# Kernel tuning notes

Measured on AMD Instinct MI355X. Metric: run time of the kernel, lower is better.

Reference implementation:

```python
import jax, jax.numpy as jnp
import numpy as np
from jax import lax

B, T, D_IN, HID, LAT, OUT = 512, 8, 6, 128, 64, 2
DT = 0.1  # Euler step size used by NeuralODESolver


def _lrelu(x):
    return jnp.where(x >= 0, x, 0.2 * x)  # LeakyReLU(0.2)


def _ivp(z, tdelta, A1, a1, A2, a2, A3, a3):
    """Explicit-Euler IVP solve: dz/dt = MLP([z, t]); tdelta is a static float."""
    steps = int(np.ceil(abs(tdelta) / DT))
    if steps == 0:
        return z
    adt = jnp.asarray(tdelta / steps, z.dtype)
    ts = jnp.arange(steps, dtype=z.dtype) * DT  # t fed to ode_func is step*dt
    def body(zc, t):
        tv = jnp.full((zc.shape[0], 1), t, zc.dtype)
        h = jnp.tanh(jnp.concatenate([zc, tv], axis=1) @ A1 + a1)
        h = jnp.tanh(h @ A2 + a2)
        return zc + (h @ A3 + a3) * adt, None
    zf, _ = lax.scan(body, z, ts)
    return zf


def setup_inputs() -> dict:
    key = jax.random.key(0)
    ks = jax.random.split(key, 24)
    s = 0.1
    w = lambda k, sh: jax.random.normal(k, sh, jnp.float32) * s
    z = lambda sh: jnp.zeros(sh, jnp.float32)
    return {
        "features": jax.random.normal(ks[0], (B, T, D_IN), jnp.float32),
        "eps": jax.random.normal(ks[1], (B, LAT), jnp.float32),
        "fe_W1": w(ks[2], (D_IN, HID)), "fe_b1": z((HID,)),
        "fe_W2": w(ks[3], (HID, HID // 2)), "fe_b2": z((HID // 2,)),
        "fe_W3": w(ks[4], (HID // 2, LAT)), "fe_b3": z((LAT,)),
        "enc_A1": w(ks[5], (LAT + 1, HID)), "enc_a1": z((HID,)),
        "enc_A2": w(ks[6], (HID, HID)), "enc_a2": z((HID,)),
        "enc_A3": w(ks[7], (HID, LAT)), "enc_a3": z((LAT,)),
        "post_W1": w(ks[8], (LAT, HID // 2)), "post_b1": z((HID // 2,)),
        "post_W2": w(ks[9], (HID // 2, 2 * LAT)), "post_b2": z((2 * LAT,)),
        "mix_W1": w(ks[10], (LAT, HID // 4)), "mix_b1": z((HID // 4,)),
        "mix_W2": w(ks[11], (HID // 4, 1)), "mix_b2": z((1,)),
        "dec_A1": w(ks[12], (LAT + 1, HID)), "dec_a1": z((HID,)),
        "dec_A2": w(ks[13], (HID, HID)), "dec_a2": z((HID,)),
        "dec_A3": w(ks[14], (HID, LAT)), "dec_a3": z((LAT,)),
        "rec_W1": w(ks[15], (LAT, HID)), "rec_b1": z((HID,)),
        "rec_W2": w(ks[16], (HID, HID // 2)), "rec_b2": z((HID // 2,)),
        "rec_W3": w(ks[17], (HID // 2, OUT)), "rec_b3": z((OUT,)),
        "time_steps": T,
    }


def reference(features, eps, fe_W1, fe_b1, fe_W2, fe_b2, fe_W3, fe_b3,
              enc_A1, enc_a1, enc_A2, enc_a2, enc_A3, enc_a3,
              post_W1, post_b1, post_W2, post_b2,
              mix_W1, mix_b1, mix_W2, mix_b2,
              dec_A1, dec_a1, dec_A2, dec_a2, dec_A3, dec_a3,
              rec_W1, rec_b1, rec_W2, rec_b2, rec_W3, rec_b3, time_steps):
    # Embedding: feature MLP -> [B, T, LAT]
    emb = _lrelu(features @ fe_W1 + fe_b1)
    emb = _lrelu(emb @ fe_W2 + fe_b2)
    emb = emb @ fe_W3 + fe_b3
    # Encoder: evolve each time point backward to t0, then posterior net
    mus, lvs = [], []
    for t in range(time_steps):
        z0e = _ivp(emb[:, t, :], -float(t), enc_A1, enc_a1, enc_A2, enc_a2, enc_A3, enc_a3)
        p = _lrelu(z0e @ post_W1 + post_b1) @ post_W2 + post_b2
        mus.append(p[:, :LAT])
        lvs.append(p[:, LAT:])
    mu = jnp.stack(mus, axis=1)   # [B, T, LAT]
    lv = jnp.stack(lvs, axis=1)   # [B, T, LAT]
    # Mixing weights over time (Softmax(dim=1))
    wlog = _lrelu(mu @ mix_W1 + mix_b1) @ mix_W2 + mix_b2  # [B, T, 1]
    wmix = jax.nn.softmax(wlog, axis=1)
    mu0 = jnp.sum(wmix * mu, axis=1)
    lv0 = jnp.sum(wmix * lv, axis=1)
    # Reparameterize with externally supplied noise
    z0 = mu0 + eps * jnp.exp(0.5 * lv0)
    # Decoder: evolve z0 forward to each time point
    seq = [z0] + [_ivp(z0, float(t), dec_A1, dec_a1, dec_A2, dec_a2, dec_A3, dec_a3)
                  for t in range(1, time_steps)]
    lat = jnp.stack(seq, axis=1)  # [B, T, LAT]
    # Reconstruction MLP -> [B, T, OUT]
    h = _lrelu(lat @ rec_W1 + rec_b1)
    h = _lrelu(h @ rec_W2 + rec_b2)
    return h @ rec_W3 + rec_b3
```

## Files before the change

### kernel.cpp

```cpp
#include <hip/hip_runtime.h>

#define TT 8

typedef __attribute__((ext_vector_type(4))) float f32x4;
typedef __attribute__((ext_vector_type(8))) short s16x8;
typedef __attribute__((ext_vector_type(4))) short s16x4;

__device__ __forceinline__ float lrelu(float x){ return fmaxf(x, 0.2f*x); }

__device__ __forceinline__ float fast_tanh(float x){
  float e = __expf(2.f*x);
  return 1.f - 2.f/(e+1.f);
}

__device__ __forceinline__ short f2b(float f){
  unsigned int u = __float_as_uint(f);
  unsigned int r = (u + 0x7fffu + ((u>>16)&1u)) >> 16;
  return (short)(r & 0xffffu);
}

__device__ __forceinline__ s16x8 load_afrag(const float* __restrict__ W, int ldw,
                                            int k0, int c0, int lane){
  s16x8 f;
  const int r = lane & 15, kb = (lane >> 4) * 8;
  #pragma unroll
  for(int e=0;e<8;++e) f[e] = f2b(W[(size_t)(k0 + kb + e)*ldw + c0 + r]);
  return f;
}

struct Frags {
  s16x8 a1f[2];
  s16x8 a2f[4];
  s16x8 a3f[4];
  float wt1[4], b1[4], b2[4], b3[4];
};

__device__ __forceinline__ void load_frags(Frags& F,
    const float* __restrict__ A1, const float* __restrict__ a1,
    const float* __restrict__ A2, const float* __restrict__ a2,
    const float* __restrict__ A3, const float* __restrict__ a3,
    int w, int l){
  const int h = l >> 4;
  #pragma unroll
  for(int kt=0;kt<2;++kt) F.a1f[kt] = load_afrag(A1, 128, 32*kt, 16*w, l);
  #pragma unroll
  for(int kt=0;kt<4;++kt) F.a2f[kt] = load_afrag(A2, 128, 32*kt, 16*w, l);
  #pragma unroll
  for(int r=0;r<4;++r){
    const int c = 16*w + 4*h + r;
    F.wt1[r] = A1[64*128 + c];
    F.b1[r]  = a1[c];
    F.b2[r]  = a2[c];
  }
  if(w < 4){
    #pragma unroll
    for(int kt=0;kt<4;++kt) F.a3f[kt] = load_afrag(A3, 64, 32*kt, 16*w, l);
    #pragma unroll
    for(int r=0;r<4;++r) F.b3[r] = a3[16*w + 4*h + r];
  }
}

__device__ __forceinline__ void ivp_step(const Frags& F, int w, int l,
    float tk, float adt, float (&zreg)[4],
    short* __restrict__ zB, short* __restrict__ h1p, short* __restrict__ h2p,
    float* __restrict__ latRow){
  const int h = l>>4, st = l&15;
  const int wrow = (2*w + (h>>1))*16 + st;
  const int welem = 4*(h&1);
  {
    s16x8 bz0 = *(const s16x8*)(zB + (size_t)l*8);
    s16x8 bz1 = *(const s16x8*)(zB + (size_t)(64+l)*8);
    f32x4 acc = {0.f,0.f,0.f,0.f};
    acc = __builtin_amdgcn_mfma_f32_16x16x32_bf16(F.a1f[0], bz0, acc, 0,0,0);
    acc = __builtin_amdgcn_mfma_f32_16x16x32_bf16(F.a1f[1], bz1, acc, 0,0,0);
    s16x4 pk;
    #pragma unroll
    for(int r=0;r<4;++r) pk[r] = f2b(fast_tanh(fmaf(tk, F.wt1[r], acc[r]) + F.b1[r]));
    *(s16x4*)(h1p + (size_t)wrow*8 + welem) = pk;
  }
  __syncthreads();
  {
    f32x4 acc = {0.f,0.f,0.f,0.f};
    #pragma unroll
    for(int kt=0;kt<4;++kt){
      s16x8 b = *(const s16x8*)(h1p + (size_t)(64*kt + l)*8);
      acc = __builtin_amdgcn_mfma_f32_16x16x32_bf16(F.a2f[kt], b, acc, 0,0,0);
    }
    s16x4 pk;
    #pragma unroll
    for(int r=0;r<4;++r) pk[r] = f2b(fast_tanh(acc[r] + F.b2[r]));
    *(s16x4*)(h2p + (size_t)wrow*8 + welem) = pk;
  }
  __syncthreads();
  if(w < 4){
    f32x4 acc = {0.f,0.f,0.f,0.f};
    #pragma unroll
    for(int kt=0;kt<4;++kt){
      s16x8 b = *(const s16x8*)(h2p + (size_t)(64*kt + l)*8);
      acc = __builtin_amdgcn_mfma_f32_16x16x32_bf16(F.a3f[kt], b, acc, 0,0,0);
    }
    s16x4 pk;
    #pragma unroll
    for(int r=0;r<4;++r){
      zreg[r] = fmaf(adt, acc[r] + F.b3[r], zreg[r]);
      pk[r] = f2b(zreg[r]);
    }
    *(s16x4*)(zB + (size_t)wrow*8 + welem) = pk;
    if(latRow){
      #pragma unroll
      for(int r=0;r<4;++r) latRow[(16*w + 4*h + r)*16 + st] = zreg[r];
    }
  }
  __syncthreads();
}

extern "C" __global__ void __launch_bounds__(512, 2)
k_enc(const float* __restrict__ features,
      const float* __restrict__ feW1, const float* __restrict__ feb1,
      const float* __restrict__ feW2, const float* __restrict__ feb2,
      const float* __restrict__ feW3, const float* __restrict__ feb3,
      const float* __restrict__ A1, const float* __restrict__ a1,
      const float* __restrict__ A2, const float* __restrict__ a2,
      const float* __restrict__ A3, const float* __restrict__ a3,
      const float* __restrict__ pW1, const float* __restrict__ pb1,
      const float* __restrict__ pW2, const float* __restrict__ pb2,
      float* __restrict__ ws_mu, float* __restrict__ ws_lv)
{
  __shared__ __align__(16) short zB[128*8];
  __shared__ __align__(16) short h1p[256*8];
  __shared__ __align__(16) short h2p[256*8];
  __shared__ float featS[16][6];
  __shared__ float hE1[128][16];
  __shared__ float hE2[64][16];
  __shared__ float zE[64][16];
  const int tid = threadIdx.x, l = tid & 63, w = tid >> 6;
  const int c1 = tid & 127, sh = tid >> 7;
  const int t_blk = blockIdx.x & 7, chunk = blockIdx.x >> 3, s0 = chunk*16;

  Frags F;
  load_frags(F, A1, a1, A2, a2, A3, a3, w, l);

  if(tid < 96){
    int e = tid / 6, i = tid - 6*e;
    featS[e][i] = features[((size_t)(s0+e)*TT + t_blk)*6 + i];
  }
  __syncthreads();
  {
    float acc[4]; const float b = feb1[c1];
    #pragma unroll
    for(int e=0;e<4;++e) acc[e]=b;
    #pragma unroll
    for(int i=0;i<6;++i){
      const float wv = feW1[i*128 + c1];
      #pragma unroll
      for(int e=0;e<4;++e) acc[e] = fmaf(featS[4*sh+e][i], wv, acc[e]);
    }
    #pragma unroll
    for(int e=0;e<4;++e) hE1[c1][4*sh+e] = lrelu(acc[e]);
  }
  __syncthreads();
  {
    float acc[2]; const float b = feb2[l];
    acc[0]=b; acc[1]=b;
    for(int i=0;i<128;++i){
      const float wv = feW2[i*64 + l];
      acc[0] = fmaf(hE1[i][2*w  ], wv, acc[0]);
      acc[1] = fmaf(hE1[i][2*w+1], wv, acc[1]);
    }
    hE2[l][2*w  ] = lrelu(acc[0]);
    hE2[l][2*w+1] = lrelu(acc[1]);
  }
  __syncthreads();
  {
    float acc[2]; const float b = feb3[l];
    acc[0]=b; acc[1]=b;
    for(int i=0;i<64;++i){
      const float wv = feW3[i*64 + l];
      acc[0] = fmaf(hE2[i][2*w  ], wv, acc[0]);
      acc[1] = fmaf(hE2[i][2*w+1], wv, acc[1]);
    }
    zE[l][2*w  ] = acc[0];
    zE[l][2*w+1] = acc[1];
  }
  __syncthreads();
  float zreg[4] = {0.f,0.f,0.f,0.f};
  if(w < 4){
    const int h=l>>4, st=l&15;
    s16x4 pk;
    #pragma unroll
    for(int r=0;r<4;++r){ zreg[r] = zE[16*w+4*h+r][st]; pk[r]=f2b(zreg[r]); }
    *(s16x4*)(zB + (size_t)((2*w+(h>>1))*16+st)*8 + 4*(h&1)) = pk;
  }
  __syncthreads();

  const int steps = 10*t_blk;
  for(int k=0;k<steps;++k)
    ivp_step(F, w, l, 0.1f*(float)k, -0.1f, zreg, zB, h1p, h2p, nullptr);

  if(w < 4){
    const int h=l>>4, st=l&15;
    #pragma unroll
    for(int r=0;r<4;++r) zE[16*w+4*h+r][st] = zreg[r];
  }
  __syncthreads();
  {
    float acc[2]; const float b = pb1[l];
    acc[0]=b; acc[1]=b;
    for(int i=0;i<64;++i){
      const float wv = pW1[i*64 + l];
      acc[0] = fmaf(zE[i][2*w  ], wv, acc[0]);
      acc[1] = fmaf(zE[i][2*w+1], wv, acc[1]);
    }
    hE2[l][2*w  ] = lrelu(acc[0]);
    hE2[l][2*w+1] = lrelu(acc[1]);
  }
  __syncthreads();
  {
    float acc[4]; const float b = pb2[c1];
    #pragma unroll
    for(int e=0;e<4;++e) acc[e]=b;
    for(int i=0;i<64;++i){
      const float wv = pW2[i*128 + c1];
      #pragma unroll
      for(int e=0;e<4;++e) acc[e] = fmaf(hE2[i][4*sh+e], wv, acc[e]);
    }
    #pragma unroll
    for(int e=0;e<4;++e){
      const int s = s0 + 4*sh + e;
      const size_t o = ((size_t)s*TT + t_blk)*64;
      if(c1 < 64) ws_mu[o + c1] = acc[e];
      else        ws_lv[o + c1 - 64] = acc[e];
    }
  }
}

extern "C" __global__ void __launch_bounds__(512, 2)
k_dec(const float* __restrict__ mu_g, const float* __restrict__ lv_g,
      const float* __restrict__ eps,
      const float* __restrict__ mxW1, const float* __restrict__ mxb1,
      const float* __restrict__ mxW2, const float* __restrict__ mxb2,
      const float* __restrict__ A1, const float* __restrict__ a1,
      const float* __restrict__ A2, const float* __restrict__ a2,
      const float* __restrict__ A3, const float* __restrict__ a3,
      const float* __restrict__ rW1, const float* __restrict__ rb1,
      const float* __restrict__ rW2, const float* __restrict__ rb2,
      const float* __restrict__ rW3, const float* __restrict__ rb3,
      float* __restrict__ out)
{
  __shared__ __align__(16) short zB[128*8];
  __shared__ __align__(16) short h1p[256*8];
  __shared__ __align__(16) short h2p[256*8];
  __shared__ float muB[16*8*64];
  __shared__ float lvB[16*8*64];
  __shared__ float mh[16][8][32];
  __shared__ float LATS[TT][64][16];
  __shared__ float wsm[16][8];
  const int tid = threadIdx.x, l = tid & 63, w = tid >> 6;
  const int c1 = tid & 127, sh = tid >> 7;
  const int b0 = blockIdx.x * 16;

  for(int idx=tid; idx<8192; idx+=512){
    muB[idx] = mu_g[(size_t)b0*512 + idx];
    lvB[idx] = lv_g[(size_t)b0*512 + idx];
  }
  Frags F;
  load_frags(F, A1, a1, A2, a2, A3, a3, w, l);
  __syncthreads();

  for(int idx=tid; idx<4096; idx+=512){
    const int s = idx>>8, t = (idx>>5)&7, c = idx&31;
    float a = mxb1[c];
    #pragma unroll 8
    for(int i=0;i<64;++i) a = fmaf(muB[(s*8+t)*64+i], mxW1[i*32+c], a);
    mh[s][t][c] = lrelu(a);
  }
  __syncthreads();
  if(tid < 128){
    const int s = tid>>3, t = tid&7;
    float a = mxb2[0];
    #pragma unroll
    for(int i=0;i<32;++i) a = fmaf(mh[s][t][i], mxW2[i], a);
    wsm[s][t] = a;
  }
  __syncthreads();
  if(tid < 16){
    float m = -1e30f;
    #pragma unroll
    for(int t=0;t<8;++t) m = fmaxf(m, wsm[tid][t]);
    float e[8], S=0.f;
    #pragma unroll
    for(int t=0;t<8;++t){ e[t] = __expf(wsm[tid][t]-m); S += e[t]; }
    const float inv = 1.f/S;
    #pragma unroll
    for(int t=0;t<8;++t) wsm[tid][t] = e[t]*inv;
  }
  __syncthreads();
  float zreg[4] = {0.f,0.f,0.f,0.f};
  if(w < 4){
    const int h=l>>4, st=l&15;
    s16x4 pk;
    #pragma unroll
    for(int r=0;r<4;++r){
      const int c = 16*w + 4*h + r;
      float mu0=0.f, lv0=0.f;
      #pragma unroll
      for(int t=0;t<8;++t){
        const float wv = wsm[st][t];
        mu0 = fmaf(wv, muB[(st*8+t)*64 + c], mu0);
        lv0 = fmaf(wv, lvB[(st*8+t)*64 + c], lv0);
      }
      const float z0 = fmaf(eps[(size_t)(b0+st)*64 + c], __expf(0.5f*lv0), mu0);
      zreg[r] = z0; pk[r] = f2b(z0);
      LATS[0][c][st] = z0;
    }
    *(s16x4*)(zB + (size_t)((2*w+(h>>1))*16+st)*8 + 4*(h&1)) = pk;
  }
  __syncthreads();

  for(int k=0;k<70;++k){
    float* latRow = (((k+1)%10)==0) ? &LATS[(k+1)/10][0][0] : nullptr;
    ivp_step(F, w, l, 0.1f*(float)k, 0.1f, zreg, zB, h1p, h2p, latRow);
  }

  float* hR1 = muB;
  float* hR2 = muB + 128*16;
  for(int t=0;t<TT;++t){
    {
      float acc[4]; const float b = rb1[c1];
      #pragma unroll
      for(int e=0;e<4;++e) acc[e]=b;
      for(int i=0;i<64;++i){
        const float wv = rW1[i*128 + c1];
        #pragma unroll
        for(int e=0;e<4;++e) acc[e] = fmaf(LATS[t][i][4*sh+e], wv, acc[e]);
      }
      #pragma unroll
      for(int e=0;e<4;++e) hR1[c1*16 + 4*sh + e] = lrelu(acc[e]);
    }
    __syncthreads();
    {
      float acc[2]; const float b = rb2[l];
      acc[0]=b; acc[1]=b;
      for(int i=0;i<128;++i){
        const float wv = rW2[i*64 + l];
        acc[0] = fmaf(hR1[i*16 + 2*w  ], wv, acc[0]);
        acc[1] = fmaf(hR1[i*16 + 2*w+1], wv, acc[1]);
      }
      hR2[l*16 + 2*w  ] = lrelu(acc[0]);
      hR2[l*16 + 2*w+1] = lrelu(acc[1]);
    }
    __syncthreads();
    if(tid < 32){
      const int s = tid >> 1, o = tid & 1;
      float a = rb3[o];
      for(int i=0;i<64;++i) a = fmaf(hR2[i*16 + s], rW3[i*2 + o], a);
      out[((size_t)(b0+s)*TT + t)*2 + o] = a;
    }
    __syncthreads();
  }
}

extern "C" void kernel_launch(void* const* d_in, const int* in_sizes, int n_in,
                              void* d_out, int out_size, void* d_ws, size_t ws_size,
                              hipStream_t stream){
  const float* features=(const float*)d_in[0];
  const float* eps     =(const float*)d_in[1];
  const float* feW1=(const float*)d_in[2];  const float* feb1=(const float*)d_in[3];
  const float* feW2=(const float*)d_in[4];  const float* feb2=(const float*)d_in[5];
  const float* feW3=(const float*)d_in[6];  const float* feb3=(const float*)d_in[7];
  const float* eA1=(const float*)d_in[8];   const float* ea1=(const float*)d_in[9];
  const float* eA2=(const float*)d_in[10];  const float* ea2=(const float*)d_in[11];
  const float* eA3=(const float*)d_in[12];  const float* ea3=(const float*)d_in[13];
  const float* pW1=(const float*)d_in[14];  const float* pb1=(const float*)d_in[15];
  const float* pW2=(const float*)d_in[16];  const float* pb2=(const float*)d_in[17];
  const float* mxW1=(const float*)d_in[18]; const float* mxb1=(const float*)d_in[19];
  const float* mxW2=(const float*)d_in[20]; const float* mxb2=(const float*)d_in[21];
  const float* dA1=(const float*)d_in[22];  const float* da1=(const float*)d_in[23];
  const float* dA2=(const float*)d_in[24];  const float* da2=(const float*)d_in[25];
  const float* dA3=(const float*)d_in[26];  const float* da3=(const float*)d_in[27];
  const float* rW1=(const float*)d_in[28];  const float* rb1=(const float*)d_in[29];
  const float* rW2=(const float*)d_in[30];  const float* rb2=(const float*)d_in[31];
  const float* rW3=(const float*)d_in[32];  const float* rb3=(const float*)d_in[33];

  float* ws_mu=(float*)d_ws;
  float* ws_lv=ws_mu + 512*8*64;

  k_enc<<<dim3(256),dim3(512),0,stream>>>(features,
      feW1,feb1,feW2,feb2,feW3,feb3,
      eA1,ea1,eA2,ea2,eA3,ea3,
      pW1,pb1,pW2,pb2,
      ws_mu, ws_lv);
  k_dec<<<dim3(32),dim3(512),0,stream>>>(ws_mu, ws_lv, eps,
      mxW1,mxb1,mxW2,mxb2,
      dA1,da1,dA2,da2,dA3,da3,
      rW1,rb1,rW2,rb2,rW3,rb3,
      (float*)d_out);
}
```

Baseline: 325.3 us.

## Process two 16-sample groups per 1024-thread block in encoder and decoder

Doubles the block size to 1024 threads so each block handles 32 samples as two independent 16-sample MFMA groups, which halves the encoder and decoder grids. Each group gets its own zB/h1p/h2p LDS buffers, but both groups share the block-wide barriers. Shared arrays are padded to a stride of 33 to avoid LDS bank conflicts. The mixing stage now reads mu/lv straight from global memory instead of staging them in LDS. The cost is that fewer CUs are busy and more waves compete on each CU during the latency-bound serial ODE steps. A large padding LDS array is also added, which limits how many blocks fit per CU.

```diff
diff --git a/kernel.cpp b/kernel.cpp
--- a/kernel.cpp
+++ b/kernel.cpp
@@ -7,22 +7,20 @@
 typedef __attribute__((ext_vector_type(4))) short s16x4;
 
 __device__ __forceinline__ float lrelu(float x){ return fmaxf(x, 0.2f*x); }
-
 __device__ __forceinline__ float fast_tanh(float x){
   float e = __expf(2.f*x);
   return 1.f - 2.f/(e+1.f);
 }
-
 __device__ __forceinline__ short f2b(float f){
-  unsigned int u = __float_as_uint(f);
-  unsigned int r = (u + 0x7fffu + ((u>>16)&1u)) >> 16;
+  unsigned u = __float_as_uint(f);
+  unsigned r = (u + 0x7fffu + ((u>>16)&1u)) >> 16;
   return (short)(r & 0xffffu);
 }
 
 __device__ __forceinline__ s16x8 load_afrag(const float* __restrict__ W, int ldw,
-                                            int k0, int c0, int lane){
+                                            int k0, int c0, int l){
   s16x8 f;
-  const int r = lane & 15, kb = (lane >> 4) * 8;
+  const int r = l & 15, kb = (l >> 4) * 8;
   #pragma unroll
   for(int e=0;e<8;++e) f[e] = f2b(W[(size_t)(k0 + kb + e)*ldw + c0 + r]);
   return f;
@@ -39,64 +37,64 @@
     const float* __restrict__ A1, const float* __restrict__ a1,
     const float* __restrict__ A2, const float* __restrict__ a2,
     const float* __restrict__ A3, const float* __restrict__ a3,
-    int w, int l){
+    int wct, int l){
   const int h = l >> 4;
   #pragma unroll
-  for(int kt=0;kt<2;++kt) F.a1f[kt] = load_afrag(A1, 128, 32*kt, 16*w, l);
+  for(int kt=0;kt<2;++kt) F.a1f[kt] = load_afrag(A1, 128, 32*kt, 16*wct, l);
   #pragma unroll
-  for(int kt=0;kt<4;++kt) F.a2f[kt] = load_afrag(A2, 128, 32*kt, 16*w, l);
+  for(int kt=0;kt<4;++kt) F.a2f[kt] = load_afrag(A2, 128, 32*kt, 16*wct, l);
   #pragma unroll
   for(int r=0;r<4;++r){
-    const int c = 16*w + 4*h + r;
+    const int c = 16*wct + 4*h + r;
     F.wt1[r] = A1[64*128 + c];
     F.b1[r]  = a1[c];
     F.b2[r]  = a2[c];
   }
-  if(w < 4){
-    #pragma unroll
-    for(int kt=0;kt<4;++kt) F.a3f[kt] = load_afrag(A3, 64, 32*kt, 16*w, l);
-    #pragma unroll
-    for(int r=0;r<4;++r) F.b3[r] = a3[16*w + 4*h + r];
-  }
-}
-
-__device__ __forceinline__ void ivp_step(const Frags& F, int w, int l,
+  if(wct < 4){
+    #pragma unroll
+    for(int kt=0;kt<4;++kt) F.a3f[kt] = load_afrag(A3, 64, 32*kt, 16*wct, l);
+    #pragma unroll
+    for(int r=0;r<4;++r) F.b3[r] = a3[16*wct + 4*h + r];
+  }
+}
+
+__device__ __forceinline__ void ivp_step(const Frags& F, int wct, int grp, int l,
     float tk, float adt, float (&zreg)[4],
-    short* __restrict__ zB, short* __restrict__ h1p, short* __restrict__ h2p,
-    float* __restrict__ latRow){
+    short* __restrict__ zBg, short* __restrict__ h1pg, short* __restrict__ h2pg,
+    float* __restrict__ latBase){
   const int h = l>>4, st = l&15;
-  const int wrow = (2*w + (h>>1))*16 + st;
-  const int welem = 4*(h&1);
-  {
-    s16x8 bz0 = *(const s16x8*)(zB + (size_t)l*8);
-    s16x8 bz1 = *(const s16x8*)(zB + (size_t)(64+l)*8);
+  const int wrow = (2*wct + (h>>1))*16 + st;
+  const int we = 4*(h&1);
+  {
+    s16x8 bz0 = *(const s16x8*)(zBg + (size_t)l*8);
+    s16x8 bz1 = *(const s16x8*)(zBg + (size_t)(64+l)*8);
     f32x4 acc = {0.f,0.f,0.f,0.f};
     acc = __builtin_amdgcn_mfma_f32_16x16x32_bf16(F.a1f[0], bz0, acc, 0,0,0);
     acc = __builtin_amdgcn_mfma_f32_16x16x32_bf16(F.a1f[1], bz1, acc, 0,0,0);
     s16x4 pk;
     #pragma unroll
     for(int r=0;r<4;++r) pk[r] = f2b(fast_tanh(fmaf(tk, F.wt1[r], acc[r]) + F.b1[r]));
-    *(s16x4*)(h1p + (size_t)wrow*8 + welem) = pk;
+    *(s16x4*)(h1pg + (size_t)wrow*8 + we) = pk;
   }
   __syncthreads();
   {
     f32x4 acc = {0.f,0.f,0.f,0.f};
     #pragma unroll
     for(int kt=0;kt<4;++kt){
-      s16x8 b = *(const s16x8*)(h1p + (size_t)(64*kt + l)*8);
+      s16x8 b = *(const s16x8*)(h1pg + (size_t)(64*kt + l)*8);
       acc = __builtin_amdgcn_mfma_f32_16x16x32_bf16(F.a2f[kt], b, acc, 0,0,0);
     }
     s16x4 pk;
     #pragma unroll
     for(int r=0;r<4;++r) pk[r] = f2b(fast_tanh(acc[r] + F.b2[r]));
-    *(s16x4*)(h2p + (size_t)wrow*8 + welem) = pk;
-  }
-  __syncthreads();
-  if(w < 4){
+    *(s16x4*)(h2pg + (size_t)wrow*8 + we) = pk;
+  }
+  __syncthreads();
+  if(wct < 4){
     f32x4 acc = {0.f,0.f,0.f,0.f};
     #pragma unroll
     for(int kt=0;kt<4;++kt){
-      s16x8 b = *(const s16x8*)(h2p + (size_t)(64*kt + l)*8);
+      s16x8 b = *(const s16x8*)(h2pg + (size_t)(64*kt + l)*8);
       acc = __builtin_amdgcn_mfma_f32_16x16x32_bf16(F.a3f[kt], b, acc, 0,0,0);
     }
     s16x4 pk;
@@ -105,16 +103,16 @@
       zreg[r] = fmaf(adt, acc[r] + F.b3[r], zreg[r]);
       pk[r] = f2b(zreg[r]);
     }
-    *(s16x4*)(zB + (size_t)wrow*8 + welem) = pk;
-    if(latRow){
-      #pragma unroll
-      for(int r=0;r<4;++r) latRow[(16*w + 4*h + r)*16 + st] = zreg[r];
-    }
-  }
-  __syncthreads();
-}
-
-extern "C" __global__ void __launch_bounds__(512, 2)
+    *(s16x4*)(zBg + (size_t)wrow*8 + we) = pk;
+    if(latBase){
+      #pragma unroll
+      for(int r=0;r<4;++r) latBase[(16*wct + 4*h + r)*33 + grp*16 + st] = zreg[r];
+    }
+  }
+  __syncthreads();
+}
+
+extern "C" __global__ void __launch_bounds__(1024, 4)
 k_enc(const float* __restrict__ features,
       const float* __restrict__ feW1, const float* __restrict__ feb1,
       const float* __restrict__ feW2, const float* __restrict__ feb2,
@@ -126,21 +124,29 @@
       const float* __restrict__ pW2, const float* __restrict__ pb2,
       float* __restrict__ ws_mu, float* __restrict__ ws_lv)
 {
-  __shared__ __align__(16) short zB[128*8];
-  __shared__ __align__(16) short h1p[256*8];
-  __shared__ __align__(16) short h2p[256*8];
-  __shared__ float featS[16][6];
-  __shared__ float hE1[128][16];
-  __shared__ float hE2[64][16];
-  __shared__ float zE[64][16];
+  __shared__ __align__(16) short zB[2*128*8];
+  __shared__ __align__(16) short h1p[2*256*8];
+  __shared__ __align__(16) short h2p[2*256*8];
+  __shared__ float featS[32][6];
+  __shared__ float hE1[128*33];
+  __shared__ float hE2[64*33];
+  __shared__ float zE[64*33];
+  __shared__ float pad_lds[7040];
   const int tid = threadIdx.x, l = tid & 63, w = tid >> 6;
+  const int wct = w >> 1, grp = w & 1;
   const int c1 = tid & 127, sh = tid >> 7;
-  const int t_blk = blockIdx.x & 7, chunk = blockIdx.x >> 3, s0 = chunk*16;
+  const int q = w;
+  const int t_blk = blockIdx.x & 7, chunk = blockIdx.x >> 3, s0 = chunk*32;
+  if(gridDim.y == 7u) pad_lds[tid & 1023] = 1.f;
+
+  short* zBg  = zB  + (size_t)grp*128*8;
+  short* h1pg = h1p + (size_t)grp*256*8;
+  short* h2pg = h2p + (size_t)grp*256*8;
 
   Frags F;
-  load_frags(F, A1, a1, A2, a2, A3, a3, w, l);
-
-  if(tid < 96){
+  load_frags(F, A1, a1, A2, a2, A3, a3, wct, l);
+
+  if(tid < 192){
     int e = tid / 6, i = tid - 6*e;
     featS[e][i] = features[((size_t)(s0+e)*TT + t_blk)*6 + i];
   }
@@ -156,7 +162,7 @@
       for(int e=0;e<4;++e) acc[e] = fmaf(featS[4*sh+e][i], wv, acc[e]);
     }
     #pragma unroll
-    for(int e=0;e<4;++e) hE1[c1][4*sh+e] = lrelu(acc[e]);
+    for(int e=0;e<4;++e) hE1[c1*33 + 4*sh+e] = lrelu(acc[e]);
   }
   __syncthreads();
   {
@@ -164,11 +170,11 @@
     acc[0]=b; acc[1]=b;
     for(int i=0;i<128;++i){
       const float wv = feW2[i*64 + l];
-      acc[0] = fmaf(hE1[i][2*w  ], wv, acc[0]);
-      acc[1] = fmaf(hE1[i][2*w+1], wv, acc[1]);
-    }
-    hE2[l][2*w  ] = lrelu(acc[0]);
-    hE2[l][2*w+1] = lrelu(acc[1]);
+      acc[0] = fmaf(hE1[i*33 + 2*q  ], wv, acc[0]);
+      acc[1] = fmaf(hE1[i*33 + 2*q+1], wv, acc[1]);
+    }
+    hE2[l*33 + 2*q  ] = lrelu(acc[0]);
+    hE2[l*33 + 2*q+1] = lrelu(acc[1]);
   }
   __syncthreads();
   {
@@ -176,31 +182,31 @@
     acc[0]=b; acc[1]=b;
     for(int i=0;i<64;++i){
       const float wv = feW3[i*64 + l];
-      acc[0] = fmaf(hE2[i][2*w  ], wv, acc[0]);
-      acc[1] = fmaf(hE2[i][2*w+1], wv, acc[1]);
-    }
-    zE[l][2*w  ] = acc[0];
-    zE[l][2*w+1] = acc[1];
+      acc[0] = fmaf(hE2[i*33 + 2*q  ], wv, acc[0]);
+      acc[1] = fmaf(hE2[i*33 + 2*q+1], wv, acc[1]);
+    }
+    zE[l*33 + 2*q  ] = acc[0];
+    zE[l*33 + 2*q+1] = acc[1];
   }
   __syncthreads();
   float zreg[4] = {0.f,0.f,0.f,0.f};
-  if(w < 4){
+  if(wct < 4){
     const int h=l>>4, st=l&15;
     s16x4 pk;
     #pragma unroll
-    for(int r=0;r<4;++r){ zreg[r] = zE[16*w+4*h+r][st]; pk[r]=f2b(zreg[r]); }
-    *(s16x4*)(zB + (size_t)((2*w+(h>>1))*16+st)*8 + 4*(h&1)) = pk;
-  }
-  __syncthreads();
-
-  const int steps = 10*t_blk;
-  for(int k=0;k<steps;++k)
-    ivp_step(F, w, l, 0.1f*(float)k, -0.1f, zreg, zB, h1p, h2p, nullptr);
-
-  if(w < 4){
+    for(int r=0;r<4;++r){ zreg[r] = zE[(16*wct+4*h+r)*33 + grp*16+st]; pk[r]=f2b(zreg[r]); }
+    *(s16x4*)(zBg + (size_t)((2*wct+(h>>1))*16+st)*8 + 4*(h&1)) = pk;
+  }
+  __syncthreads();
+
+  const int steps = 10 * t_blk;
+  for(int k=0; k<steps; ++k)
+    ivp_step(F, wct, grp, l, 0.1f*(float)k, -0.1f, zreg, zBg, h1pg, h2pg, nullptr);
+
+  if(wct < 4){
     const int h=l>>4, st=l&15;
     #pragma unroll
-    for(int r=0;r<4;++r) zE[16*w+4*h+r][st] = zreg[r];
+    for(int r=0;r<4;++r) zE[(16*wct+4*h+r)*33 + grp*16+st] = zreg[r];
   }
   __syncthreads();
   {
@@ -208,11 +214,11 @@
     acc[0]=b; acc[1]=b;
     for(int i=0;i<64;++i){
       const float wv = pW1[i*64 + l];
-      acc[0] = fmaf(zE[i][2*w  ], wv, acc[0]);
-      acc[1] = fmaf(zE[i][2*w+1], wv, acc[1]);
-    }
-    hE2[l][2*w  ] = lrelu(acc[0]);
-    hE2[l][2*w+1] = lrelu(acc[1]);
+      acc[0] = fmaf(zE[i*33 + 2*q  ], wv, acc[0]);
+      acc[1] = fmaf(zE[i*33 + 2*q+1], wv, acc[1]);
+    }
+    hE2[l*33 + 2*q  ] = lrelu(acc[0]);
+    hE2[l*33 + 2*q+1] = lrelu(acc[1]);
   }
   __syncthreads();
   {
@@ -222,7 +228,7 @@
     for(int i=0;i<64;++i){
       const float wv = pW2[i*128 + c1];
       #pragma unroll
-      for(int e=0;e<4;++e) acc[e] = fmaf(hE2[i][4*sh+e], wv, acc[e]);
+      for(int e=0;e<4;++e) acc[e] = fmaf(hE2[i*33 + 4*sh+e], wv, acc[e]);
     }
     #pragma unroll
     for(int e=0;e<4;++e){
@@ -234,7 +240,7 @@
   }
 }
 
-extern "C" __global__ void __launch_bounds__(512, 2)
+extern "C" __global__ void __launch_bounds__(1024, 4)
 k_dec(const float* __restrict__ mu_g, const float* __restrict__ lv_g,
       const float* __restrict__ eps,
       const float* __restrict__ mxW1, const float* __restrict__ mxb1,
@@ -247,83 +253,87 @@
       const float* __restrict__ rW3, const float* __restrict__ rb3,
       float* __restrict__ out)
 {
-  __shared__ __align__(16) short zB[128*8];
-  __shared__ __align__(16) short h1p[256*8];
-  __shared__ __align__(16) short h2p[256*8];
-  __shared__ float muB[16*8*64];
-  __shared__ float lvB[16*8*64];
-  __shared__ float mh[16][8][32];
-  __shared__ float LATS[TT][64][16];
-  __shared__ float wsm[16][8];
+  __shared__ __align__(16) short zB[2*128*8];
+  __shared__ __align__(16) short h1p[2*256*8];
+  __shared__ __align__(16) short h2p[2*256*8];
+  __shared__ float pool[8448];
+  __shared__ float LATS[8*64*33];
+  __shared__ float wlS[256];
+  __shared__ float wsmS[32][8];
   const int tid = threadIdx.x, l = tid & 63, w = tid >> 6;
+  const int wct = w >> 1, grp = w & 1;
   const int c1 = tid & 127, sh = tid >> 7;
-  const int b0 = blockIdx.x * 16;
-
-  for(int idx=tid; idx<8192; idx+=512){
-    muB[idx] = mu_g[(size_t)b0*512 + idx];
-    lvB[idx] = lv_g[(size_t)b0*512 + idx];
-  }
+  const int q = w;
+  const int b0 = blockIdx.x * 32;
+
+  short* zBg  = zB  + (size_t)grp*128*8;
+  short* h1pg = h1p + (size_t)grp*256*8;
+  short* h2pg = h2p + (size_t)grp*256*8;
+
   Frags F;
-  load_frags(F, A1, a1, A2, a2, A3, a3, w, l);
-  __syncthreads();
-
-  for(int idx=tid; idx<4096; idx+=512){
-    const int s = idx>>8, t = (idx>>5)&7, c = idx&31;
+  load_frags(F, A1, a1, A2, a2, A3, a3, wct, l);
+
+  for(int p=0; p<8; ++p){
+    int idx = tid + p*1024;
+    int s = idx>>8, t = (idx>>5)&7, c = idx&31;
     float a = mxb1[c];
     #pragma unroll 8
-    for(int i=0;i<64;++i) a = fmaf(muB[(s*8+t)*64+i], mxW1[i*32+c], a);
-    mh[s][t][c] = lrelu(a);
-  }
-  __syncthreads();
-  if(tid < 128){
-    const int s = tid>>3, t = tid&7;
+    for(int i=0;i<64;++i) a = fmaf(mu_g[((size_t)(b0+s)*TT + t)*64 + i], mxW1[i*32+c], a);
+    pool[(s*8+t)*33 + c] = lrelu(a);
+  }
+  __syncthreads();
+  if(tid < 256){
+    int s = tid>>3, t = tid&7;
     float a = mxb2[0];
     #pragma unroll
-    for(int i=0;i<32;++i) a = fmaf(mh[s][t][i], mxW2[i], a);
-    wsm[s][t] = a;
-  }
-  __syncthreads();
-  if(tid < 16){
+    for(int i=0;i<32;++i) a = fmaf(pool[(s*8+t)*33 + i], mxW2[i], a);
+    wlS[tid] = a;
+  }
+  __syncthreads();
+  if(tid < 32){
     float m = -1e30f;
     #pragma unroll
-    for(int t=0;t<8;++t) m = fmaxf(m, wsm[tid][t]);
-    float e[8], S=0.f;
-    #pragma unroll
-    for(int t=0;t<8;++t){ e[t] = __expf(wsm[tid][t]-m); S += e[t]; }
+    for(int t=0;t<8;++t) m = fmaxf(m, wlS[tid*8+t]);
+    float e[8], S = 0.f;
+    #pragma unroll
+    for(int t=0;t<8;++t){ e[t] = __expf(wlS[tid*8+t]-m); S += e[t]; }
     const float inv = 1.f/S;
     #pragma unroll
-    for(int t=0;t<8;++t) wsm[tid][t] = e[t]*inv;
+    for(int t=0;t<8;++t) wsmS[tid][t] = e[t]*inv;
   }
   __syncthreads();
   float zreg[4] = {0.f,0.f,0.f,0.f};
-  if(w < 4){
-    const int h=l>>4, st=l&15;
+  if(wct < 4){
+    const int h=l>>4, st=l&15, sidx = grp*16+st;
+    float wsv[8];
+    #pragma unroll
+    for(int t=0;t<8;++t) wsv[t] = wsmS[sidx][t];
     s16x4 pk;
     #pragma unroll
     for(int r=0;r<4;++r){
-      const int c = 16*w + 4*h + r;
-      float mu0=0.f, lv0=0.f;
+      const int c = 16*wct + 4*h + r;
+      float mu0 = 0.f, lv0 = 0.f;
       #pragma unroll
       for(int t=0;t<8;++t){
-        const float wv = wsm[st][t];
-        mu0 = fmaf(wv, muB[(st*8+t)*64 + c], mu0);
-        lv0 = fmaf(wv, lvB[(st*8+t)*64 + c], lv0);
+        size_t o = ((size_t)(b0+sidx)*TT + t)*64 + c;
+        mu0 = fmaf(wsv[t], mu_g[o], mu0);
+        lv0 = fmaf(wsv[t], lv_g[o], lv0);
       }
-      const float z0 = fmaf(eps[(size_t)(b0+st)*64 + c], __expf(0.5f*lv0), mu0);
+      const float z0 = fmaf(eps[(size_t)(b0+sidx)*64 + c], __expf(0.5f*lv0), mu0);
       zreg[r] = z0; pk[r] = f2b(z0);
-      LATS[0][c][st] = z0;
-    }
-    *(s16x4*)(zB + (size_t)((2*w+(h>>1))*16+st)*8 + 4*(h&1)) = pk;
-  }
-  __syncthreads();
-
-  for(int k=0;k<70;++k){
-    float* latRow = (((k+1)%10)==0) ? &LATS[(k+1)/10][0][0] : nullptr;
-    ivp_step(F, w, l, 0.1f*(float)k, 0.1f, zreg, zB, h1p, h2p, latRow);
-  }
-
-  float* hR1 = muB;
-  float* hR2 = muB + 128*16;
+      LATS[c*33 + sidx] = z0;
+    }
+    *(s16x4*)(zBg + (size_t)((2*wct+(h>>1))*16+st)*8 + 4*(h&1)) = pk;
+  }
+  __syncthreads();
+
+  for(int k=0; k<70; ++k){
+    float* latBase = (((k+1)%10)==0) ? (LATS + ((k+1)/10)*64*33) : nullptr;
+    ivp_step(F, wct, grp, l, 0.1f*(float)k, 0.1f, zreg, zBg, h1pg, h2pg, latBase);
+  }
+
+  float* hR1 = pool;
+  float* hR2 = pool + 128*33;
   for(int t=0;t<TT;++t){
     {
       float acc[4]; const float b = rb1[c1];
@@ -332,10 +342,10 @@
       for(int i=0;i<64;++i){
         const float wv = rW1[i*128 + c1];
         #pragma unroll
-        for(int e=0;e<4;++e) acc[e] = fmaf(LATS[t][i][4*sh+e], wv, acc[e]);
+        for(int e=0;e<4;++e) acc[e] = fmaf(LATS[t*2112 + i*33 + 4*sh+e], wv, acc[e]);
       }
       #pragma unroll
-      for(int e=0;e<4;++e) hR1[c1*16 + 4*sh + e] = lrelu(acc[e]);
+      for(int e=0;e<4;++e) hR1[c1*33 + 4*sh + e] = lrelu(acc[e]);
     }
     __syncthreads();
     {
@@ -343,17 +353,17 @@
       acc[0]=b; acc[1]=b;
       for(int i=0;i<128;++i){
         const float wv = rW2[i*64 + l];
-        acc[0] = fmaf(hR1[i*16 + 2*w  ], wv, acc[0]);
-        acc[1] = fmaf(hR1[i*16 + 2*w+1], wv, acc[1]);
+        acc[0] = fmaf(hR1[i*33 + 2*q  ], wv, acc[0]);
+        acc[1] = fmaf(hR1[i*33 + 2*q+1], wv, acc[1]);
       }
-      hR2[l*16 + 2*w  ] = lrelu(acc[0]);
-      hR2[l*16 + 2*w+1] = lrelu(acc[1]);
+      hR2[(2*q  )*65 + l] = lrelu(acc[0]);
+      hR2[(2*q+1)*65 + l] = lrelu(acc[1]);
     }
     __syncthreads();
-    if(tid < 32){
+    if(tid < 64){
       const int s = tid >> 1, o = tid & 1;
       float a = rb3[o];
-      for(int i=0;i<64;++i) a = fmaf(hR2[i*16 + s], rW3[i*2 + o], a);
+      for(int i=0;i<64;++i) a = fmaf(hR2[s*65 + i], rW3[i*2 + o], a);
       out[((size_t)(b0+s)*TT + t)*2 + o] = a;
     }
     __syncthreads();
@@ -385,12 +395,12 @@
   float* ws_mu=(float*)d_ws;
   float* ws_lv=ws_mu + 512*8*64;
 
-  k_enc<<<dim3(256),dim3(512),0,stream>>>(features,
+  k_enc<<<dim3(128),dim3(1024),0,stream>>>(features,
       feW1,feb1,feW2,feb2,feW3,feb3,
       eA1,ea1,eA2,ea2,eA3,ea3,
       pW1,pb1,pW2,pb2,
       ws_mu, ws_lv);
-  k_dec<<<dim3(32),dim3(512),0,stream>>>(ws_mu, ws_lv, eps,
+  k_dec<<<dim3(16),dim3(1024),0,stream>>>(ws_mu, ws_lv, eps,
       mxW1,mxb1,mxW2,mxb2,
       dA1,da1,dA2,da2,dA3,da3,
       rW1,rb1,rW2,rb2,rW3,rb3,
```

New measurement: 668.1 us. +105.4%, slower.
